# Performance work log

Hardware: AMD Instinct MI355X
Metric: run time of the kernel (lower is better)

Reference implementation:

```python
import jax, jax.numpy as jnp
import numpy as np

D_MODEL = 1024
N_HEADS = 16
HEAD_DIM = D_MODEL // N_HEADS
ROPE_THETA = 10000.0
B, T = 2, 2048


def apply_rope(x, pos):
    # x: (b, h, t, k), pos: (b, t) int
    k = x.shape[-1]
    inv_freq = 1.0 / (ROPE_THETA ** (jnp.arange(0, k, 2, dtype=jnp.float32) / k))  # (k/2,)
    ang = pos[:, None, :, None].astype(jnp.float32) * inv_freq  # (b, 1, t, k/2)
    cos, sin = jnp.cos(ang).astype(x.dtype), jnp.sin(ang).astype(x.dtype)
    x1, x2 = x[..., 0::2], x[..., 1::2]
    r1 = x1 * cos - x2 * sin
    r2 = x1 * sin + x2 * cos
    return jnp.stack([r1, r2], axis=-1).reshape(x.shape)


def setup_inputs() -> dict:
    key = jax.random.key(0)
    ks = jax.random.split(key, 5)
    scale = 1.0 / np.sqrt(D_MODEL)
    x = jax.random.normal(ks[0], (B, T, D_MODEL), dtype=jnp.float32)
    token_positions = jnp.broadcast_to(jnp.arange(T, dtype=jnp.int64), (B, T))
    Wq = jax.random.normal(ks[1], (D_MODEL, D_MODEL), dtype=jnp.float32) * scale
    Wk = jax.random.normal(ks[2], (D_MODEL, D_MODEL), dtype=jnp.float32) * scale
    Wv = jax.random.normal(ks[3], (D_MODEL, D_MODEL), dtype=jnp.float32) * scale
    Wo = jax.random.normal(ks[4], (D_MODEL, D_MODEL), dtype=jnp.float32) * scale
    return {"x": x, "token_positions": token_positions, "Wq": Wq, "Wk": Wk, "Wv": Wv, "Wo": Wo}


def reference(x, token_positions, Wq, Wk, Wv, Wo):
    b, t, _ = x.shape
    h, k = N_HEADS, HEAD_DIM
    # Linear stores weight as (out, in): y = x @ W.T
    def proj(W):
        y = jnp.einsum('bti,oi->bto', x, W)
        return y.reshape(b, t, h, k).transpose(0, 2, 1, 3)  # (b, h, t, k)
    Q, K, V = proj(Wq), proj(Wk), proj(Wv)
    Q = apply_rope(Q, token_positions)
    K = apply_rope(K, token_positions)
    scores = jnp.einsum('bhqk,bhtk->bhqt', Q, K) / jnp.sqrt(jnp.asarray(k, x.dtype))
    causal = jnp.tril(jnp.ones((t, t), dtype=bool))
    scores = jnp.where(causal, scores, jnp.asarray(-jnp.inf, scores.dtype))
    attn = jax.nn.softmax(scores, axis=-1)
    out = jnp.einsum('bhqt,bhtk->bhqk', attn, V)  # (b, h, t, k)
    out = out.transpose(0, 2, 1, 3).reshape(b, t, h * k)
    return jnp.einsum('bti,oi->bto', out, Wo)
```

## Files before the change

### kernel.cpp

```cpp
#include <hip/hip_runtime.h>
#include <math.h>
#include <stdint.h>

#define D_MODEL 1024
#define T_SEQ   2048
#define BATCH   2
#define NH      16
#define HD      64

typedef __attribute__((ext_vector_type(8))) short bf16x8;
typedef __attribute__((ext_vector_type(4))) float f32x4;

__device__ inline unsigned short f2bf(float f) {
  union { float f; unsigned int u; } v; v.f = f;
  unsigned int u = v.u;
  unsigned int r = u + 0x7fffu + ((u >> 16) & 1u);
  return (unsigned short)(r >> 16);
}
__device__ inline float bf2f(unsigned short s) {
  union { unsigned int u; float f; } v; v.u = ((unsigned int)s) << 16;
  return v.f;
}

#define GLDS16(g, l) __builtin_amdgcn_global_load_lds( \
  reinterpret_cast<const __attribute__((address_space(1))) void*>(reinterpret_cast<uintptr_t>(g)), \
  reinterpret_cast<__attribute__((address_space(3))) void*>(reinterpret_cast<uintptr_t>(l)), 16, 0, 0)

#define PSTORE(va_, p0_, p1_, p2_, p3_) do { \
  unsigned t0_, t1_; \
  asm volatile( \
    "v_cvt_pk_bf16_f32 %0, %3, %4\n\t" \
    "v_cvt_pk_bf16_f32 %1, %5, %6\n\t" \
    "ds_write_b16 %2, %0\n\t" \
    "ds_write_b16_d16_hi %2, %0 offset:144\n\t" \
    "ds_write_b16 %2, %1 offset:288\n\t" \
    "ds_write_b16_d16_hi %2, %1 offset:432" \
    : "=&v"(t0_), "=&v"(t1_) \
    : "v"(va_), "v"(p0_), "v"(p1_), "v"(p2_), "v"(p3_) \
    : "memory"); \
} while (0)

__global__ void cast5_kernel(const float* __restrict__ x,
                             const float* __restrict__ w0, const float* __restrict__ w1,
                             const float* __restrict__ w2, const float* __restrict__ w3,
                             unsigned short* __restrict__ xb,
                             unsigned short* __restrict__ d0, unsigned short* __restrict__ d1,
                             unsigned short* __restrict__ d2, unsigned short* __restrict__ d3) {
  int id = blockIdx.x * blockDim.x + threadIdx.x;
  const float* s; unsigned short* dd; int r;
  if (id < (1 << 20)) { s = x; dd = xb; r = id; }
  else {
    int t = id - (1 << 20);
    int m = t >> 18; r = t & ((1 << 18) - 1);
    s  = (m == 0) ? w0 : (m == 1) ? w1 : (m == 2) ? w2 : w3;
    dd = (m == 0) ? d0 : (m == 1) ? d1 : (m == 2) ? d2 : d3;
  }
  float4 v = ((const float4*)s)[r];
  ushort4 o;
  o.x = f2bf(v.x); o.y = f2bf(v.y); o.z = f2bf(v.z); o.w = f2bf(v.w);
  ((ushort4*)dd)[r] = o;
}

template<int BN, bool F32OUT, bool ROPE>
__global__ __launch_bounds__(256, 3)
void gemm_bt(const unsigned short* __restrict__ A,
             const unsigned short* __restrict__ B0, const unsigned short* __restrict__ B1,
             const unsigned short* __restrict__ B2,
             void* __restrict__ C0, void* __restrict__ C1, void* __restrict__ C2,
             const int* __restrict__ pos, int M, int K) {
  constexpr int NPM = 1024 / BN;
  constexpr int NWC = BN / 64;
  constexpr int MI  = 2 * NWC;
  constexpr int NGB = BN / 8;
  __shared__ __align__(16) unsigned char As[16 * 1024];
  __shared__ __align__(16) unsigned char Bs[NGB * 1024];

  const int tid = threadIdx.x, lane = tid & 63, wid = tid >> 6;
  const int wr = wid / NWC, wc = wid % NWC;
  const int bx = blockIdx.x;
  const int mat = bx / NPM;
  const int bn = (bx % NPM) * BN;
  const int bm = blockIdx.y * 128;
  const unsigned short* B = (mat == 0) ? B0 : (mat == 1) ? B1 : B2;
  void* C = (mat == 0) ? C0 : (mat == 1) ? C1 : C2;

  f32x4 acc[MI][4];
#pragma unroll
  for (int i = 0; i < MI; i++)
#pragma unroll
    for (int j = 0; j < 4; j++) acc[i][j] = (f32x4){0.f, 0.f, 0.f, 0.f};

  const int fr = lane & 15, fg = lane >> 4;
  const int srow = lane >> 3;
  const int scg  = ((lane & 7) ^ (srow & 7)) * 8;
  const int rx   = (fr & 7) << 4;

  for (int kb = 0; kb < K; kb += 64) {
#pragma unroll
    for (int c = 0; c < 4; ++c) {
      int g = wid * 4 + c;
      GLDS16(A + (size_t)(bm + g * 8 + srow) * K + kb + scg, As + g * 1024);
    }
#pragma unroll
    for (int c = 0; c < NGB / 4; ++c) {
      int g = wid * (NGB / 4) + c;
      GLDS16(B + (size_t)(bn + g * 8 + srow) * K + kb + scg, Bs + g * 1024);
    }
    __syncthreads();
#pragma unroll
    for (int h = 0; h < 2; ++h) {
      const int co = (h * 64 + fg * 16) ^ rx;
      bf16x8 a[MI], bq[4];
#pragma unroll
      for (int mi = 0; mi < MI; mi++)
        a[mi] = *(const bf16x8*)(As + (wr * MI + mi) * 2048 + fr * 128 + co);
#pragma unroll
      for (int ni = 0; ni < 4; ni++)
        bq[ni] = *(const bf16x8*)(Bs + (wc * 4 + ni) * 2048 + fr * 128 + co);
#pragma unroll
      for (int mi = 0; mi < MI; mi++)
#pragma unroll
        for (int ni = 0; ni < 4; ni++)
          acc[mi][ni] = __builtin_amdgcn_mfma_f32_16x16x32_bf16(a[mi], bq[ni], acc[mi][ni], 0, 0, 0);
    }
    __syncthreads();
  }

  const int fc = lane & 15, fq = lane >> 4;

  if (ROPE && mat <= 1) {
    const float C1 = -0.4152410118609203f;
    const float INV2PI = 0.15915494309189535f;
    const float scl = (mat == 0) ? 0.18033688011f : 1.0f;
    float inv[4];
#pragma unroll
    for (int ni = 0; ni < 4; ++ni) {
      int p = ((ni * 16 + fc) >> 1) & 31;
      inv[ni] = __builtin_amdgcn_exp2f(C1 * (float)p) * INV2PI;
    }
    const float sgn = (fc & 1) ? 1.0f : -1.0f;
#pragma unroll
    for (int mi = 0; mi < MI; ++mi)
#pragma unroll
      for (int r = 0; r < 4; ++r) {
        int row = bm + wr * (16 * MI) + mi * 16 + fq * 4 + r;
        float posf = (float)pos[row];
#pragma unroll
        for (int ni = 0; ni < 4; ++ni) {
          float v = acc[mi][ni][r];
          float partner = __shfl_xor(v, 1);
          float rev = posf * inv[ni];
          rev = __builtin_amdgcn_fractf(rev);
          float sn, cs;
          asm("v_sin_f32 %0, %1" : "=v"(sn) : "v"(rev));
          asm("v_cos_f32 %0, %1" : "=v"(cs) : "v"(rev));
          acc[mi][ni][r] = (v * cs + partner * sn * sgn) * scl;
        }
      }
  }

#pragma unroll
  for (int mi = 0; mi < MI; mi++)
#pragma unroll
    for (int ni = 0; ni < 4; ni++) {
      int col = bn + wc * 64 + ni * 16 + fc;
#pragma unroll
      for (int r = 0; r < 4; r++) {
        int row = bm + wr * (16 * MI) + mi * 16 + fq * 4 + r;
        if (F32OUT) ((float*)C)[(size_t)row * 1024 + col] = acc[mi][ni][r];
        else ((unsigned short*)C)[(size_t)row * 1024 + col] = f2bf(acc[mi][ni][r]);
      }
    }
}

__global__ __launch_bounds__(256, 3)
void attn_kernel(const unsigned short* __restrict__ Q, const unsigned short* __restrict__ K,
                 const unsigned short* __restrict__ V, unsigned short* __restrict__ O) {
  __shared__ __align__(16) unsigned char KsRaw[2][8192];
  __shared__ __align__(16) unsigned char VtRaw[2][8192];
  __shared__ __align__(16) unsigned char PsRaw[4][2304];

  const int lin  = (int)blockIdx.x;
  const int xcd  = lin & 7;
  const int slot = lin >> 3;
  const int pr   = slot & 15;
  const int bh   = ((slot >> 4) << 3) | xcd;
  const int b  = bh >> 4, h = bh & 15;
  const int tid = threadIdx.x, lane = tid & 63, wid = tid >> 6;
  const int fr = lane & 15, fg = lane >> 4;

  const size_t base = ((size_t)b * T_SEQ) * D_MODEL + h * HD;
  const unsigned short* Qb = Q + base;
  const unsigned short* Kb = K + base;
  const unsigned short* Vb = V + base;

  const int qt0 = pr, qt1 = 31 - pr;
  const int ntkA = pr + 1;
  const int ntkB = 32 - pr;

  bf16x8 qfA0, qfA1, qfB0, qfB1;
  {
    const unsigned short* qp0 = Qb + (size_t)(qt0 * 64 + wid * 16 + fr) * D_MODEL + fg * 8;
    qfA0 = *(const bf16x8*)qp0;  qfA1 = *(const bf16x8*)(qp0 + 32);
    const unsigned short* qp1 = Qb + (size_t)(qt1 * 64 + wid * 16 + fr) * D_MODEL + fg * 8;
    qfB0 = *(const bf16x8*)qp1;  qfB1 = *(const bf16x8*)(qp1 + 32);
  }

  const int sg  = tid >> 3;
  const int sd0 = (tid & 7) * 8;
  const int sx  = tid & 7;

#define STAGE_K(kvbase, buf) do { \
    _Pragma("unroll") \
    for (int c_ = 0; c_ < 2; ++c_) { \
      int idx_ = wid * 2 + c_; \
      int nt_ = idx_ >> 1, hf_ = idx_ & 1; \
      GLDS16(Kb + (size_t)((kvbase) + nt_ * 16 + fr) * D_MODEL + hf_ * 32 + fg * 8, \
             &KsRaw[buf][idx_ * 1024]); \
    } \
  } while (0)

#define STAGE_V_WRITE(ra_, rb_, bufp_) do { \
    _Pragma("unroll") \
    for (int j_ = 0; j_ < 8; ++j_) { \
      unsigned pk_ = (unsigned)(unsigned short)(ra_)[j_] | ((unsigned)(unsigned short)(rb_)[j_] << 16); \
      *(unsigned*)((bufp_) + (sd0 + j_) * 128 + ((sg * 4) ^ ((j_ ^ sx) << 4))) = pk_; \
    } \
  } while (0)

  STAGE_K(0, 0);
  {
    bf16x8 ra = *(const bf16x8*)(Vb + (size_t)(2 * sg    ) * D_MODEL + sd0);
    bf16x8 rb = *(const bf16x8*)(Vb + (size_t)(2 * sg + 1) * D_MODEL + sd0);
    STAGE_V_WRITE(ra, rb, &VtRaw[0][0]);
  }

  unsigned pva[4];
  {
    unsigned psb = (unsigned)(uintptr_t)(void*)&PsRaw[wid][0];
#pragma unroll
    for (int nt = 0; nt < 4; ++nt)
      pva[nt] = psb + fg * 576 + (unsigned)((nt * 32 + fr * 2) ^ (fg << 5));
  }

  float m_run[4], l_part[4];
  f32x4 acc[4];
#pragma unroll
  for (int r = 0; r < 4; ++r) { m_run[r] = -INFINITY; l_part[r] = 0.f; }
#pragma unroll
  for (int d = 0; d < 4; ++d) acc[d] = (f32x4){0.f, 0.f, 0.f, 0.f};

#define UNIT(qt_, kt_, qlo_, qhi_, par_, hn_, kvn_) do { \
    __syncthreads(); \
    bf16x8 nva, nvb; \
    if (hn_) { \
      STAGE_K(kvn_, (par_) ^ 1); \
      nva = *(const bf16x8*)(Vb + (size_t)((kvn_) + 2 * sg    ) * D_MODEL + sd0); \
      nvb = *(const bf16x8*)(Vb + (size_t)((kvn_) + 2 * sg + 1) * D_MODEL + sd0); \
    } \
    const unsigned char* kbuf = &KsRaw[par_][0]; \
    f32x4 st[4]; \
    __builtin_amdgcn_s_setprio(1); \
    _Pragma("unroll") \
    for (int nt = 0; nt < 4; ++nt) { \
      bf16x8 kf0 = *(const bf16x8*)(kbuf + (nt * 2    ) * 1024 + lane * 16); \
      bf16x8 kf1 = *(const bf16x8*)(kbuf + (nt * 2 + 1) * 1024 + lane * 16); \
      f32x4 sa = (f32x4){0.f, 0.f, 0.f, 0.f}; \
      sa = __builtin_amdgcn_mfma_f32_16x16x32_bf16(qlo_, kf0, sa, 0, 0, 0); \
      sa = __builtin_amdgcn_mfma_f32_16x16x32_bf16(qhi_, kf1, sa, 0, 0, 0); \
      st[nt] = sa; \
    } \
    __builtin_amdgcn_s_setprio(0); \
    float p[4][4]; \
    _Pragma("unroll") \
    for (int nt = 0; nt < 4; ++nt) \
      _Pragma("unroll") \
      for (int r = 0; r < 4; ++r) p[nt][r] = st[nt][r]; \
    if ((kt_) == (qt_)) {    \
      _Pragma("unroll") \
      for (int nt = 0; nt < 4; ++nt) { \
        _Pragma("unroll") \
        for (int r = 0; r < 4; ++r) \
          if (nt * 16 + fr > wid * 16 + fg * 4 + r) p[nt][r] = -INFINITY; \
      } \
    } \
    float lmax[4]; \
    bool ok = true; \
    _Pragma("unroll") \
    for (int r = 0; r < 4; ++r) { \
      lmax[r] = fmaxf(fmaxf(p[0][r], p[1][r]), fmaxf(p[2][r], p[3][r])); \
      ok = ok && (lmax[r] <= m_run[r] + 8.0f); \
    } \
    if (!__all(ok)) { \
      _Pragma("unroll") \
      for (int r = 0; r < 4; ++r) { \
        float tm = lmax[r]; \
        tm = fmaxf(tm, __shfl_xor(tm, 1)); \
        tm = fmaxf(tm, __shfl_xor(tm, 2)); \
        tm = fmaxf(tm, __shfl_xor(tm, 4)); \
        tm = fmaxf(tm, __shfl_xor(tm, 8)); \
        float mn = fmaxf(m_run[r], tm); \
        float sc = __builtin_amdgcn_exp2f(m_run[r] - mn); \
        m_run[r] = mn; \
        l_part[r] *= sc; \
        _Pragma("unroll") \
        for (int d = 0; d < 4; ++d) acc[d][r] *= sc; \
      } \
    } \
    _Pragma("unroll") \
    for (int nt = 0; nt < 4; ++nt) { \
      float pv0 = __builtin_amdgcn_exp2f(p[nt][0] - m_run[0]); \
      float pv1 = __builtin_amdgcn_exp2f(p[nt][1] - m_run[1]); \
      float pv2 = __builtin_amdgcn_exp2f(p[nt][2] - m_run[2]); \
      float pv3 = __builtin_amdgcn_exp2f(p[nt][3] - m_run[3]); \
      l_part[0] += pv0; l_part[1] += pv1; l_part[2] += pv2; l_part[3] += pv3; \
      PSTORE(pva[nt], pv0, pv1, pv2, pv3); \
    } \
    asm volatile("s_waitcnt lgkmcnt(0)" ::: "memory"); \
    __builtin_amdgcn_sched_barrier(0); \
    bf16x8 pa0 = *(const bf16x8*)(&PsRaw[wid][0] + fr * 144 + ((     fg * 16) ^ ((fr >> 2) << 5))); \
    bf16x8 pa1 = *(const bf16x8*)(&PsRaw[wid][0] + fr * 144 + ((64 + fg * 16) ^ ((fr >> 2) << 5))); \
    const unsigned char* vbuf = &VtRaw[par_][0]; \
    __builtin_amdgcn_s_setprio(1); \
    _Pragma("unroll") \
    for (int dblk = 0; dblk < 4; ++dblk) { \
      int xr = ((fr & 7) ^ ((dblk * 2 + (fr >> 3)) & 7)) << 4; \
      const unsigned char* vp = vbuf + (dblk * 16 + fr) * 128; \
      bf16x8 b0 = *(const bf16x8*)(vp + ((fg * 16) ^ xr)); \
      bf16x8 b1 = *(const bf16x8*)(vp + ((64 + fg * 16) ^ xr)); \
      acc[dblk] = __builtin_amdgcn_mfma_f32_16x16x32_bf16(pa0, b0, acc[dblk], 0, 0, 0); \
      acc[dblk] = __builtin_amdgcn_mfma_f32_16x16x32_bf16(pa1, b1, acc[dblk], 0, 0, 0); \
    } \
    __builtin_amdgcn_s_setprio(0); \
    if (hn_) STAGE_V_WRITE(nva, nvb, &VtRaw[(par_) ^ 1][0]); \
  } while (0)

#define EPILOGUE(qt_) do { \
    _Pragma("unroll") \
    for (int r = 0; r < 4; ++r) { \
      float l = l_part[r]; \
      l += __shfl_xor(l, 1); l += __shfl_xor(l, 2); \
      l += __shfl_xor(l, 4); l += __shfl_xor(l, 8); \
      float rl = __builtin_amdgcn_rcpf(l); \
      int row = (qt_) * 64 + wid * 16 + fg * 4 + r; \
      unsigned short* orow = O + ((size_t)b * T_SEQ + row) * D_MODEL + h * HD; \
      _Pragma("unroll") \
      for (int d = 0; d < 4; ++d) orow[d * 16 + fr] = f2bf(acc[d][r] * rl); \
    } \
  } while (0)

  int par = 0;
  for (int kt = 0; kt < ntkA; ++kt) {
    int kvn = (kt + 1 < ntkA) ? (kt + 1) * 64 : 0;
    UNIT(qt0, kt, qfA0, qfA1, par, true, kvn);
    par ^= 1;
  }
  EPILOGUE(qt0);
#pragma unroll
  for (int r = 0; r < 4; ++r) { m_run[r] = -INFINITY; l_part[r] = 0.f; }
#pragma unroll
  for (int d = 0; d < 4; ++d) acc[d] = (f32x4){0.f, 0.f, 0.f, 0.f};
  for (int kt = 0; kt < ntkB; ++kt) {
    bool hn = (kt + 1 < ntkB);
    int kvn = (kt + 1) * 64;
    UNIT(qt1, kt, qfB0, qfB1, par, hn, kvn);
    par ^= 1;
  }
  EPILOGUE(qt1);
#undef UNIT
#undef EPILOGUE
#undef STAGE_K
#undef STAGE_V_WRITE
}

extern "C" void kernel_launch(void* const* d_in, const int* in_sizes, int n_in,
                              void* d_out, int out_size, void* d_ws, size_t ws_size,
                              hipStream_t stream) {
  const float* x   = (const float*)d_in[0];
  const int*   pos = (const int*)d_in[1];
  const float* Wq  = (const float*)d_in[2];
  const float* Wk  = (const float*)d_in[3];
  const float* Wv  = (const float*)d_in[4];
  const float* Wo  = (const float*)d_in[5];

  const size_t M  = (size_t)BATCH * T_SEQ;
  const size_t DD = (size_t)D_MODEL * D_MODEL;

  char* ws = (char*)d_ws;
  unsigned short* xb  = (unsigned short*)ws; ws += M * D_MODEL * 2;
  unsigned short* Wqb = (unsigned short*)ws; ws += DD * 2;
  unsigned short* Wkb = (unsigned short*)ws; ws += DD * 2;
  unsigned short* Wvb = (unsigned short*)ws; ws += DD * 2;
  unsigned short* Wob = (unsigned short*)ws; ws += DD * 2;
  unsigned short* Qp  = (unsigned short*)ws; ws += M * D_MODEL * 2;
  unsigned short* Kp  = (unsigned short*)ws; ws += M * D_MODEL * 2;
  unsigned short* Vp  = (unsigned short*)ws; ws += M * D_MODEL * 2;
  unsigned short* Ob  = (unsigned short*)ws; ws += M * D_MODEL * 2;

  cast5_kernel<<<8192, 256, 0, stream>>>(x, Wq, Wk, Wv, Wo, xb, Wqb, Wkb, Wvb, Wob);

  gemm_bt<128, false, true><<<dim3(24, (unsigned)(M / 128)), 256, 0, stream>>>(
      xb, Wqb, Wkb, Wvb, Qp, Kp, Vp, pos, (int)M, D_MODEL);

  attn_kernel<<<dim3(512), 256, 0, stream>>>(Qp, Kp, Vp, Ob);

  gemm_bt<64, true, false><<<dim3(16, (unsigned)(M / 128)), 256, 0, stream>>>(
      Ob, Wob, Wob, Wob, d_out, d_out, d_out, nullptr, (int)M, D_MODEL);
}
```

Baseline: 104.1 us.

## Process 128-row KV tiles per barrier with two 64-row subtiles in attention

The attention loop now stages 128 KV rows of K and V per double-buffered iteration and processes them as two 64-row subtiles, skipping the second when it lies fully above the causal diagonal. This halves the number of __syncthreads and staging rounds per query tile, giving more work between barriers. In exchange LDS use roughly doubles and launch bounds drop from 3 to 2 blocks per CU, which lowers occupancy. Some K/V rows beyond the causal limit may be loaded without being used.

After: 104.1 us. Within noise of the previous version (+0.0%).

```diff
diff --git a/kernel.cpp b/kernel.cpp
--- a/kernel.cpp
+++ b/kernel.cpp
@@ -173,11 +173,11 @@
     }
 }
 
-__global__ __launch_bounds__(256, 3)
+__global__ __launch_bounds__(256, 2)
 void attn_kernel(const unsigned short* __restrict__ Q, const unsigned short* __restrict__ K,
                  const unsigned short* __restrict__ V, unsigned short* __restrict__ O) {
-  __shared__ __align__(16) unsigned char KsRaw[2][8192];
-  __shared__ __align__(16) unsigned char VtRaw[2][8192];
+  __shared__ __align__(16) unsigned char KsRaw[2][16384];
+  __shared__ __align__(16) unsigned char VtRaw[2][2][8192];
   __shared__ __align__(16) unsigned char PsRaw[4][2304];
 
   const int lin  = (int)blockIdx.x;
@@ -195,8 +195,8 @@
   const unsigned short* Vb = V + base;
 
   const int qt0 = pr, qt1 = 31 - pr;
-  const int ntkA = pr + 1;
-  const int ntkB = 32 - pr;
+  const int uA = (pr + 2) >> 1;
+  const int uB = (33 - pr) >> 1;
 
   bf16x8 qfA0, qfA1, qfB0, qfB1;
   {
@@ -210,12 +210,12 @@
   const int sd0 = (tid & 7) * 8;
   const int sx  = tid & 7;
 
-#define STAGE_K(kvbase, buf) do { \
-    _Pragma("unroll") \
-    for (int c_ = 0; c_ < 2; ++c_) { \
-      int idx_ = wid * 2 + c_; \
-      int nt_ = idx_ >> 1, hf_ = idx_ & 1; \
-      GLDS16(Kb + (size_t)((kvbase) + nt_ * 16 + fr) * D_MODEL + hf_ * 32 + fg * 8, \
+#define STAGE_K128(kvbase, buf) do { \
+    _Pragma("unroll") \
+    for (int c_ = 0; c_ < 4; ++c_) { \
+      int idx_ = wid * 4 + c_; \
+      int kv16_ = idx_ >> 1, hf_ = idx_ & 1; \
+      GLDS16(Kb + (size_t)((kvbase) + kv16_ * 16 + fr) * D_MODEL + hf_ * 32 + fg * 8, \
              &KsRaw[buf][idx_ * 1024]); \
     } \
   } while (0)
@@ -228,11 +228,14 @@
     } \
   } while (0)
 
-  STAGE_K(0, 0);
+  STAGE_K128(0, 0);
   {
-    bf16x8 ra = *(const bf16x8*)(Vb + (size_t)(2 * sg    ) * D_MODEL + sd0);
-    bf16x8 rb = *(const bf16x8*)(Vb + (size_t)(2 * sg + 1) * D_MODEL + sd0);
-    STAGE_V_WRITE(ra, rb, &VtRaw[0][0]);
+    bf16x8 ra = *(const bf16x8*)(Vb + (size_t)(2 * sg     ) * D_MODEL + sd0);
+    bf16x8 rb = *(const bf16x8*)(Vb + (size_t)(2 * sg + 1 ) * D_MODEL + sd0);
+    bf16x8 rc = *(const bf16x8*)(Vb + (size_t)(64 + 2 * sg    ) * D_MODEL + sd0);
+    bf16x8 rd = *(const bf16x8*)(Vb + (size_t)(64 + 2 * sg + 1) * D_MODEL + sd0);
+    STAGE_V_WRITE(ra, rb, &VtRaw[0][0][0]);
+    STAGE_V_WRITE(rc, rd, &VtRaw[0][1][0]);
   }
 
   unsigned pva[4];
@@ -250,15 +253,8 @@
 #pragma unroll
   for (int d = 0; d < 4; ++d) acc[d] = (f32x4){0.f, 0.f, 0.f, 0.f};
 
-#define UNIT(qt_, kt_, qlo_, qhi_, par_, hn_, kvn_) do { \
-    __syncthreads(); \
-    bf16x8 nva, nvb; \
-    if (hn_) { \
-      STAGE_K(kvn_, (par_) ^ 1); \
-      nva = *(const bf16x8*)(Vb + (size_t)((kvn_) + 2 * sg    ) * D_MODEL + sd0); \
-      nvb = *(const bf16x8*)(Vb + (size_t)((kvn_) + 2 * sg + 1) * D_MODEL + sd0); \
-    } \
-    const unsigned char* kbuf = &KsRaw[par_][0]; \
+#define SUBTILE(qt_, kv64_, s_, qlo_, qhi_, par_) do { \
+    const unsigned char* kbuf = &KsRaw[par_][(s_) * 8192]; \
     f32x4 st[4]; \
     __builtin_amdgcn_s_setprio(1); \
     _Pragma("unroll") \
@@ -276,7 +272,7 @@
     for (int nt = 0; nt < 4; ++nt) \
       _Pragma("unroll") \
       for (int r = 0; r < 4; ++r) p[nt][r] = st[nt][r]; \
-    if ((kt_) == (qt_)) {    \
+    if ((kv64_) == (qt_)) {    \
       _Pragma("unroll") \
       for (int nt = 0; nt < 4; ++nt) { \
         _Pragma("unroll") \
@@ -320,7 +316,7 @@
     __builtin_amdgcn_sched_barrier(0); \
     bf16x8 pa0 = *(const bf16x8*)(&PsRaw[wid][0] + fr * 144 + ((     fg * 16) ^ ((fr >> 2) << 5))); \
     bf16x8 pa1 = *(const bf16x8*)(&PsRaw[wid][0] + fr * 144 + ((64 + fg * 16) ^ ((fr >> 2) << 5))); \
-    const unsigned char* vbuf = &VtRaw[par_][0]; \
+    const unsigned char* vbuf = &VtRaw[par_][s_][0]; \
     __builtin_amdgcn_s_setprio(1); \
     _Pragma("unroll") \
     for (int dblk = 0; dblk < 4; ++dblk) { \
@@ -332,7 +328,25 @@
       acc[dblk] = __builtin_amdgcn_mfma_f32_16x16x32_bf16(pa1, b1, acc[dblk], 0, 0, 0); \
     } \
     __builtin_amdgcn_s_setprio(0); \
-    if (hn_) STAGE_V_WRITE(nva, nvb, &VtRaw[(par_) ^ 1][0]); \
+  } while (0)
+
+#define UNIT128(qt_, u_, qlo_, qhi_, par_, hn_, kvn_) do { \
+    __syncthreads(); \
+    bf16x8 nva0, nvb0, nva1, nvb1; \
+    if (hn_) { \
+      STAGE_K128(kvn_, (par_) ^ 1); \
+      nva0 = *(const bf16x8*)(Vb + (size_t)((kvn_) + 2 * sg     ) * D_MODEL + sd0); \
+      nvb0 = *(const bf16x8*)(Vb + (size_t)((kvn_) + 2 * sg + 1 ) * D_MODEL + sd0); \
+      nva1 = *(const bf16x8*)(Vb + (size_t)((kvn_) + 64 + 2 * sg    ) * D_MODEL + sd0); \
+      nvb1 = *(const bf16x8*)(Vb + (size_t)((kvn_) + 64 + 2 * sg + 1) * D_MODEL + sd0); \
+    } \
+    SUBTILE(qt_, 2 * (u_), 0, qlo_, qhi_, par_); \
+    if (2 * (u_) + 1 <= (qt_)) \
+      SUBTILE(qt_, 2 * (u_) + 1, 1, qlo_, qhi_, par_); \
+    if (hn_) { \
+      STAGE_V_WRITE(nva0, nvb0, &VtRaw[(par_) ^ 1][0][0]); \
+      STAGE_V_WRITE(nva1, nvb1, &VtRaw[(par_) ^ 1][1][0]); \
+    } \
   } while (0)
 
 #define EPILOGUE(qt_) do { \
@@ -350,9 +364,9 @@
   } while (0)
 
   int par = 0;
-  for (int kt = 0; kt < ntkA; ++kt) {
-    int kvn = (kt + 1 < ntkA) ? (kt + 1) * 64 : 0;
-    UNIT(qt0, kt, qfA0, qfA1, par, true, kvn);
+  for (int u = 0; u < uA; ++u) {
+    int kvn = (u + 1 < uA) ? (u + 1) * 128 : 0;
+    UNIT128(qt0, u, qfA0, qfA1, par, true, kvn);
     par ^= 1;
   }
   EPILOGUE(qt0);
@@ -360,16 +374,16 @@
   for (int r = 0; r < 4; ++r) { m_run[r] = -INFINITY; l_part[r] = 0.f; }
 #pragma unroll
   for (int d = 0; d < 4; ++d) acc[d] = (f32x4){0.f, 0.f, 0.f, 0.f};
-  for (int kt = 0; kt < ntkB; ++kt) {
-    bool hn = (kt + 1 < ntkB);
-    int kvn = (kt + 1) * 64;
-    UNIT(qt1, kt, qfB0, qfB1, par, hn, kvn);
+  for (int u = 0; u < uB; ++u) {
+    bool hn = (u + 1 < uB);
+    UNIT128(qt1, u, qfB0, qfB1, par, hn, (u + 1) * 128);
     par ^= 1;
   }
   EPILOGUE(qt1);
-#undef UNIT
+#undef UNIT128
+#undef SUBTILE
 #undef EPILOGUE
-#undef STAGE_K
+#undef STAGE_K128
 #undef STAGE_V_WRITE
 }
 
```

## Split paired causal query tiles into separate blocks with heavy-first scheduling

Applied to the files above, without the earlier changes.

Each attention block previously handled two query tiles (pr and 31-pr) so every block did equal causal work. Now each block handles a single query tile, the grid doubles to 1024 blocks, and the block-index-to-tile mapping issues the heaviest tiles in the first round and lighter ones later, interleaving across XCDs and heads. This exposes more parallelism and shortens each block's serial chain, at the cost of uneven per-block work and reloading K/V per block instead of reusing staging across the pair.

New measurement: 99.57 us (median of 3 runs). 4.3% less time.

```diff
diff --git a/kernel.cpp b/kernel.cpp
--- a/kernel.cpp
+++ b/kernel.cpp
@@ -180,11 +180,13 @@
   __shared__ __align__(16) unsigned char VtRaw[2][8192];
   __shared__ __align__(16) unsigned char PsRaw[4][2304];
 
-  const int lin  = (int)blockIdx.x;
-  const int xcd  = lin & 7;
-  const int slot = lin >> 3;
-  const int pr   = slot & 15;
-  const int bh   = ((slot >> 4) << 3) | xcd;
+  const int lin = (int)blockIdx.x;
+  const int xcd = lin & 7;
+  const int cu  = (lin >> 3) & 31;
+  const int rnd = lin >> 8;
+  const int k4  = cu >> 2;
+  const int bh  = xcd | ((cu & 3) << 3);
+  const int qt  = (rnd == 0) ? 31 - k4 : (rnd == 1) ? 16 + k4 : (rnd == 2) ? 15 - k4 : k4;
   const int b  = bh >> 4, h = bh & 15;
   const int tid = threadIdx.x, lane = tid & 63, wid = tid >> 6;
   const int fr = lane & 15, fg = lane >> 4;
@@ -194,16 +196,12 @@
   const unsigned short* Kb = K + base;
   const unsigned short* Vb = V + base;
 
-  const int qt0 = pr, qt1 = 31 - pr;
-  const int ntkA = pr + 1;
-  const int ntkB = 32 - pr;
-
-  bf16x8 qfA0, qfA1, qfB0, qfB1;
+  const int ntk = qt + 1;
+
+  bf16x8 qf0, qf1;
   {
-    const unsigned short* qp0 = Qb + (size_t)(qt0 * 64 + wid * 16 + fr) * D_MODEL + fg * 8;
-    qfA0 = *(const bf16x8*)qp0;  qfA1 = *(const bf16x8*)(qp0 + 32);
-    const unsigned short* qp1 = Qb + (size_t)(qt1 * 64 + wid * 16 + fr) * D_MODEL + fg * 8;
-    qfB0 = *(const bf16x8*)qp1;  qfB1 = *(const bf16x8*)(qp1 + 32);
+    const unsigned short* qp = Qb + (size_t)(qt * 64 + wid * 16 + fr) * D_MODEL + fg * 8;
+    qf0 = *(const bf16x8*)qp;  qf1 = *(const bf16x8*)(qp + 32);
   }
 
   const int sg  = tid >> 3;
@@ -250,7 +248,7 @@
 #pragma unroll
   for (int d = 0; d < 4; ++d) acc[d] = (f32x4){0.f, 0.f, 0.f, 0.f};
 
-#define UNIT(qt_, kt_, qlo_, qhi_, par_, hn_, kvn_) do { \
+#define UNIT(kt_, par_, hn_, kvn_) do { \
     __syncthreads(); \
     bf16x8 nva, nvb; \
     if (hn_) { \
@@ -266,8 +264,8 @@
       bf16x8 kf0 = *(const bf16x8*)(kbuf + (nt * 2    ) * 1024 + lane * 16); \
       bf16x8 kf1 = *(const bf16x8*)(kbuf + (nt * 2 + 1) * 1024 + lane * 16); \
       f32x4 sa = (f32x4){0.f, 0.f, 0.f, 0.f}; \
-      sa = __builtin_amdgcn_mfma_f32_16x16x32_bf16(qlo_, kf0, sa, 0, 0, 0); \
-      sa = __builtin_amdgcn_mfma_f32_16x16x32_bf16(qhi_, kf1, sa, 0, 0, 0); \
+      sa = __builtin_amdgcn_mfma_f32_16x16x32_bf16(qf0, kf0, sa, 0, 0, 0); \
+      sa = __builtin_amdgcn_mfma_f32_16x16x32_bf16(qf1, kf1, sa, 0, 0, 0); \
       st[nt] = sa; \
     } \
     __builtin_amdgcn_s_setprio(0); \
@@ -276,7 +274,7 @@
     for (int nt = 0; nt < 4; ++nt) \
       _Pragma("unroll") \
       for (int r = 0; r < 4; ++r) p[nt][r] = st[nt][r]; \
-    if ((kt_) == (qt_)) {    \
+    if ((kt_) == qt) {    \
       _Pragma("unroll") \
       for (int nt = 0; nt < 4; ++nt) { \
         _Pragma("unroll") \
@@ -335,40 +333,25 @@
     if (hn_) STAGE_V_WRITE(nva, nvb, &VtRaw[(par_) ^ 1][0]); \
   } while (0)
 
-#define EPILOGUE(qt_) do { \
-    _Pragma("unroll") \
-    for (int r = 0; r < 4; ++r) { \
-      float l = l_part[r]; \
-      l += __shfl_xor(l, 1); l += __shfl_xor(l, 2); \
-      l += __shfl_xor(l, 4); l += __shfl_xor(l, 8); \
-      float rl = __builtin_amdgcn_rcpf(l); \
-      int row = (qt_) * 64 + wid * 16 + fg * 4 + r; \
-      unsigned short* orow = O + ((size_t)b * T_SEQ + row) * D_MODEL + h * HD; \
-      _Pragma("unroll") \
-      for (int d = 0; d < 4; ++d) orow[d * 16 + fr] = f2bf(acc[d][r] * rl); \
-    } \
-  } while (0)
-
   int par = 0;
-  for (int kt = 0; kt < ntkA; ++kt) {
-    int kvn = (kt + 1 < ntkA) ? (kt + 1) * 64 : 0;
-    UNIT(qt0, kt, qfA0, qfA1, par, true, kvn);
+  for (int kt = 0; kt < ntk; ++kt) {
+    bool hn = (kt + 1 < ntk);
+    UNIT(kt, par, hn, (kt + 1) * 64);
     par ^= 1;
   }
-  EPILOGUE(qt0);
-#pragma unroll
-  for (int r = 0; r < 4; ++r) { m_run[r] = -INFINITY; l_part[r] = 0.f; }
-#pragma unroll
-  for (int d = 0; d < 4; ++d) acc[d] = (f32x4){0.f, 0.f, 0.f, 0.f};
-  for (int kt = 0; kt < ntkB; ++kt) {
-    bool hn = (kt + 1 < ntkB);
-    int kvn = (kt + 1) * 64;
-    UNIT(qt1, kt, qfB0, qfB1, par, hn, kvn);
-    par ^= 1;
-  }
-  EPILOGUE(qt1);
+
+#pragma unroll
+  for (int r = 0; r < 4; ++r) {
+    float l = l_part[r];
+    l += __shfl_xor(l, 1); l += __shfl_xor(l, 2);
+    l += __shfl_xor(l, 4); l += __shfl_xor(l, 8);
+    float rl = __builtin_amdgcn_rcpf(l);
+    int row = qt * 64 + wid * 16 + fg * 4 + r;
+    unsigned short* orow = O + ((size_t)b * T_SEQ + row) * D_MODEL + h * HD;
+#pragma unroll
+    for (int d = 0; d < 4; ++d) orow[d * 16 + fr] = f2bf(acc[d][r] * rl);
+  }
 #undef UNIT
-#undef EPILOGUE
 #undef STAGE_K
 #undef STAGE_V_WRITE
 }
@@ -402,7 +385,7 @@
   gemm_bt<128, false, true><<<dim3(24, (unsigned)(M / 128)), 256, 0, stream>>>(
       xb, Wqb, Wkb, Wvb, Qp, Kp, Vp, pos, (int)M, D_MODEL);
 
-  attn_kernel<<<dim3(512), 256, 0, stream>>>(Qp, Kp, Vp, Ob);
+  attn_kernel<<<dim3(1024), 256, 0, stream>>>(Qp, Kp, Vp, Ob);
 
   gemm_bt<64, true, false><<<dim3(16, (unsigned)(M / 128)), 256, 0, stream>>>(
       Ob, Wob, Wob, Wob, d_out, d_out, d_out, nullptr, (int)M, D_MODEL);
```
